# Performance work log

Measured on AMD Instinct MI355X. Metric: run time of the kernel, lower is better.

The kernel has to match this reference:

```python
import jax, jax.numpy as jnp
from jax import lax
import numpy as np

BETA, TAU, NUM_ITER = 0.33, 1.0, 5
DN = ('NCDHW', 'OIDHW', 'NCDHW')


def _base_kernels():
    # 3x3x3 neighborhood-counting kernels from the torch module
    K_N6 = np.zeros((3, 3, 3), np.float32)
    for c in [(1, 1, 0), (1, 1, 2), (1, 0, 1), (1, 2, 1), (0, 1, 1), (2, 1, 1)]:
        K_N6[c] = 1.0
    K_N26 = np.ones((3, 3, 3), np.float32); K_N26[1, 1, 1] = 0.0
    K_N18 = K_N26.copy()
    for c in [(0, 0, 0), (0, 0, 2), (0, 2, 0), (0, 2, 2), (2, 0, 0), (2, 0, 2), (2, 2, 0), (2, 2, 2)]:
        K_N18[c] = 0.0
    K_B26 = np.zeros((3, 3, 3), np.float32)
    K_B26[0, 0, 0] = 1.0
    for c in [(0, 0, 1), (0, 1, 0), (0, 1, 1), (1, 0, 0), (1, 0, 1), (1, 1, 0)]:
        K_B26[c] = -1.0
    K_A6 = np.zeros((3, 3, 3), np.float32)
    K_A6[0, 1, 1] = -1.0
    for c in [(0, 0, 1), (0, 1, 0), (0, 1, 2), (0, 2, 1)]:
        K_A6[c] = 1.0
    return K_N6, K_N26, K_N18, K_B26, K_A6


def _stacked_weight():
    # Fuse all 17 simple-check convolutions into one conv over a 3-channel input
    # channel 0: img, channel 1: 1-img, channel 2: 2*img-1
    K_N6, K_N26, K_N18, K_B26, K_A6 = _base_kernels()
    b26 = [K_B26] + [np.flip(K_B26, ax) for ax in [(0,), (1,), (2,), (0, 1), (0, 2), (1, 2), (0, 1, 2)]]
    fA = np.flip(K_A6, 0)
    a6 = [K_A6, np.rot90(K_A6, axes=(0, 1)), np.rot90(K_A6, axes=(0, 2)),
          fA, np.rot90(fA, axes=(0, 1)), np.rot90(fA, axes=(0, 2))]
    rows = []
    def put(k, ch):
        w = np.zeros((3, 3, 3, 3), np.float32)
        w[ch] = k
        rows.append(w)
    put(K_N6, 1)   # counts bg 6-neighbors (applied to 1-img)
    put(K_N26, 0)  # counts fg 26-neighbors
    put(K_N18, 0)  # counts fg 18-neighbors
    for k in b26:
        put(k, 2)  # 8 B26-cell detectors on 2*img-1
    for k in a6:
        put(k, 2)  # 6 A6-cell detectors on 2*img-1
    return jnp.asarray(np.stack(rows)), jnp.asarray(K_N26).reshape(1, 1, 3, 3, 3)


W_SIMPLE, W_N26 = _stacked_weight()


def _clip01(x):  # F.hardtanh(x, 0, 1)
    return jnp.clip(x, 0.0, 1.0)


def _endpoint_check(img):
    p = jnp.pad(img, ((0, 0), (0, 0), (1, 1), (1, 1), (1, 1)))
    n26 = lax.conv_general_dilated(p, W_N26, (1, 1, 1), 'VALID', dimension_numbers=DN)
    return _clip01(2.0 - n26)  # endpoint iff <=1 fg 26-neighbor


def _simple_check(img):
    p = jnp.pad(img, ((0, 0), (0, 0), (1, 1), (1, 1), (1, 1)))
    x3 = jnp.concatenate([p, 1.0 - p, 2.0 * p - 1.0], axis=1)
    f = lax.conv_general_dilated(x3, W_SIMPLE, (2, 2, 2), 'VALID', dimension_numbers=DN)
    n6, n26, n18 = f[:, 0:1], f[:, 1:2], f[:, 2:3]
    num_b26 = jax.nn.relu(f[:, 3:11] - 6.0).sum(axis=1, keepdims=True)
    num_a6 = jax.nn.relu(f[:, 11:17] - 4.0).sum(axis=1, keepdims=True)
    cond1 = _clip01(n6) * _clip01(2.0 - n6)                              # exactly one bg 6-neighbor
    cond2 = _clip01(n26) * _clip01(2.0 - n26)                            # exactly one fg 26-neighbor
    cond3 = _clip01(n18) * _clip01(2.0 - n18) * _clip01(1.0 - num_b26)   # one 18-neighbor, no B26 cell
    cond4 = _clip01(n6 - 1.0) * _clip01(1.0 - num_a6) * _clip01(1.0 - num_b26)  # >=2 bg 6-nb, no A6/B26 cell
    return _clip01(cond1 + cond2 + cond3 + cond4)


def _forward(img):
    # _prepare_input: zero-pad each spatial dim by 1
    img = jnp.pad(img, ((0, 0), (0, 0), (1, 1), (1, 1), (1, 1)))
    # _stochastic_discretization (reparametrization + straight-through)
    alpha = (img + 1e-8) / (1.0 - img + 1e-8)
    u = jax.random.uniform(jax.random.key(42), img.shape, img.dtype, 1e-8, 1.0 - 1e-8)
    noise = jnp.log(u) - jnp.log1p(-u)
    soft = jax.nn.sigmoid((jnp.log(alpha) + noise * BETA) / TAU)
    img = lax.stop_gradient((soft > 0.5).astype(soft.dtype) - soft) + soft
    offsets = [(0, 0, 0), (1, 0, 0), (0, 1, 0), (1, 1, 0), (0, 0, 1), (1, 0, 1), (0, 1, 1), (1, 1, 1)]
    for _ in range(NUM_ITER):
        is_end = _endpoint_check(img)
        for xo, yo, zo in offsets:
            is_simple = _simple_check(img[:, :, xo:, yo:, zo:])
            sl = (slice(None), slice(None), slice(xo, None, 2), slice(yo, None, 2), slice(zo, None, 2))
            del_cand = is_simple * (1.0 - is_end[sl])
            img = img.at[sl].set(jnp.minimum(img[sl], 1.0 - del_cand))
    # _prepare_output: strip padding
    return img[:, :, 1:-1, 1:-1, 1:-1]


def setup_inputs():
    key = jax.random.key(0)
    img = jax.random.uniform(key, (2, 1, 160, 160, 160), jnp.float32)  # probabilities in [0,1)
    return {"img": img}


def reference(img):
    return _forward(img)
```

## Files before the change

kernel.cpp:

```cpp
#include <hip/hip_runtime.h>
#include <stdint.h>

#pragma clang fp contract(off)

#define PDIM 162
#define NW   (2*PDIM*PDIM*3)
#define NWH  (NW/2)
#define OD   160

#define PZ 97
#define LADDR(lz,ly) ((lz)*PZ + (ly)*3)

__device__ __forceinline__ uint32_t rotl32(uint32_t x, uint32_t r) {
  return (x << r) | (x >> (32u - r));
}

__device__ __forceinline__ uint32_t threefry_bits(uint32_t idx) {
  const uint32_t ks0 = 0u, ks1 = 42u, ks2 = 0x1BD11BDAu ^ 0u ^ 42u;
  uint32_t x0 = 0u + ks0;
  uint32_t x1 = idx + ks1;
#define TFR(r) { x0 += x1; x1 = rotl32(x1, (r)); x1 ^= x0; }
  TFR(13u) TFR(15u) TFR(26u) TFR(6u)
  x0 += ks1; x1 += ks2 + 1u;
  TFR(17u) TFR(29u) TFR(16u) TFR(24u)
  x0 += ks2; x1 += ks0 + 2u;
  TFR(13u) TFR(15u) TFR(26u) TFR(6u)
  x0 += ks0; x1 += ks1 + 3u;
  TFR(17u) TFR(29u) TFR(16u) TFR(24u)
  x0 += ks1; x1 += ks2 + 4u;
  TFR(13u) TFR(15u) TFR(26u) TFR(6u)
  x0 += ks2; x1 += ks0 + 5u;
#undef TFR
  return x0 ^ x1;
}

__device__ __forceinline__ float xla_logf(float xin) {
  uint32_t bits = __float_as_uint(xin);
  float e = (float)((int)(bits >> 23) - 126);
  float x = __uint_as_float((bits & 0x007fffffu) | 0x3f000000u);
  const float SQRTHF = 0.707106781186547524f;
  bool lt = (x < SQRTHF);
  float tmp = lt ? x : 0.0f;
  e = e - (lt ? 1.0f : 0.0f);
  x = x - 1.0f;
  x = x + tmp;
  float z = x * x;
  float y = 7.0376836292e-2f;
  y = fmaf(y, x, -1.1514610310e-1f);
  y = fmaf(y, x,  1.1676998740e-1f);
  y = fmaf(y, x, -1.2420140846e-1f);
  y = fmaf(y, x,  1.4249322787e-1f);
  y = fmaf(y, x, -1.6668057665e-1f);
  y = fmaf(y, x,  2.0000714765e-1f);
  y = fmaf(y, x, -2.4999993993e-1f);
  y = fmaf(y, x,  3.3333331174e-1f);
  y = y * x;
  y = y * z;
  y = fmaf(e, -2.12194440e-4f, y);
  y = fmaf(-0.5f, z, y);
  x = x + y;
  x = fmaf(e, 0.693359375f, x);
  return x;
}

__device__ __forceinline__ float xla_log1pf(float x) {
  float for_large = xla_logf(x + 1.0f);
  float for_small = fmaf(-0.5f, x, 1.0f) * x;
  return (fabsf(x) < 1e-4f) ? for_small : for_large;
}

__device__ __forceinline__ bool bin_pred(const float* __restrict__ in, uint32_t w,
                                         uint32_t lane) {
  uint32_t row = w / 3u, wx = w - row * 3u;
  uint32_t n  = row / (uint32_t)(PDIM * PDIM);
  uint32_t rr = row - n * (uint32_t)(PDIM * PDIM);
  uint32_t z  = rr / (uint32_t)PDIM;
  uint32_t y  = rr - z * (uint32_t)PDIM;
  uint32_t x  = wx * 64u + lane;
  if ((z - 1u) >= 160u || (y - 1u) >= 160u || (x - 1u) >= 160u) return false;
  float v = in[((n * 160u + (z - 1u)) * 160u + (y - 1u)) * 160u + (x - 1u)];
  uint32_t i = row * 162u + x;
  uint32_t b = threefry_bits(i);
  float f  = __uint_as_float((b >> 9) | 0x3f800000u) - 1.0f;
  float uu = fmaxf(1e-8f, f + 1e-8f);
  float h  = (v + 1e-8f) / ((1.0f - v) + 1e-8f);
  const float T = 1.1920928955078125e-7f;

  const float LN2 = 0.6931471805599453f;
  float la_f = __builtin_amdgcn_logf(h) * LN2;
  float nz_f = (__builtin_amdgcn_logf(uu) - __builtin_amdgcn_logf(1.0f - uu)) * LN2;
  float zs_f = fmaf(nz_f, 0.33f, la_f);
  if (fabsf(zs_f - T) > 3.0e-4f) return zs_f > T;

  float la = xla_logf(h);
  float noise = xla_logf(uu) - xla_log1pf(-uu);
  float zs = la + noise * 0.33f;
  return zs > T;
}

__global__ __launch_bounds__(256) void k_binarize(const float* __restrict__ in,
                                                  uint64_t* __restrict__ bits) {
  uint32_t t = blockIdx.x * 256u + threadIdx.x;
  uint32_t w0 = t >> 6, lane = t & 63u;
  if (w0 >= (uint32_t)NWH) return;
  uint32_t w1 = w0 + (uint32_t)NWH;
  bool p0 = bin_pred(in, w0, lane);
  bool p1 = bin_pred(in, w1, lane);
  uint64_t m0 = __ballot(p0);
  uint64_t m1 = __ballot(p1);
  if (lane == 0) { bits[w0] = m0; bits[w1] = m1; }
}

#define NB(dz,dy,dx) ((dx)==-1 ? Lb[(dz)+1][(dy)+1] : ((dx)==1 ? Rb[(dz)+1][(dy)+1] : Vv[(dz)+1][(dy)+1]))

#define GATHER_W(SRC, lz, ly, w) \
  _Pragma("unroll") \
  for (int dz = 0; dz < 3; ++dz) \
    _Pragma("unroll") \
    for (int dy = 0; dy < 3; ++dy) { \
      int rb = LADDR((lz) + dz - 1, (ly) + dy - 1); \
      uint64_t r0 = SRC[rb], r1 = SRC[rb + 1], r2 = SRC[rb + 2]; \
      uint64_t b = ((w) == 0) ? r0 : (((w) == 1) ? r1 : r2); \
      uint64_t a = ((w) == 0) ? 0ull : (((w) == 1) ? r0 : r1); \
      uint64_t d = ((w) == 0) ? r1 : (((w) == 1) ? r2 : 0ull); \
      Vv[dz][dy] = b; \
      Lb[dz][dy] = (b << 1) | (a >> 63); \
      Rb[dz][dy] = (b >> 1) | (d << 63); \
    }

struct OG { uint64_t o, g; };
__device__ __forceinline__ OG og_leaf2(uint64_t a, uint64_t b) {
  OG r; r.o = a | b; r.g = a & b; return r;
}
__device__ __forceinline__ OG og_comb(OG a, OG b) {
  OG r; r.g = a.g | b.g | (a.o & b.o); r.o = a.o | b.o; return r;
}

#define OG_BUILD_18_C(og18, ogc) \
  OG a0 = og_leaf2(NB(-1,0,0), NB(1,0,0)); \
  OG a1 = og_leaf2(NB(0,-1,0), NB(0,1,0)); \
  OG a2 = og_leaf2(NB(0,0,-1), NB(0,0,1)); \
  OG e0 = og_leaf2(NB(-1,-1,0), NB(-1,1,0)); \
  OG e1 = og_leaf2(NB(-1,0,-1), NB(-1,0,1)); \
  OG e2 = og_leaf2(NB(1,-1,0),  NB(1,1,0)); \
  OG e3 = og_leaf2(NB(1,0,-1),  NB(1,0,1)); \
  OG e4 = og_leaf2(NB(0,-1,-1), NB(0,-1,1)); \
  OG e5 = og_leaf2(NB(0,1,-1),  NB(0,1,1)); \
  OG t0 = og_comb(a0, a1); \
  OG t1 = og_comb(a2, e0); \
  OG t2 = og_comb(e1, e2); \
  OG t3 = og_comb(e3, e4); \
  OG og18 = og_comb(og_comb(og_comb(t0, t1), og_comb(t2, t3)), e5); \
  OG c0 = og_leaf2(NB(-1,-1,-1), NB(-1,-1,1)); \
  OG c1 = og_leaf2(NB(-1,1,-1),  NB(-1,1,1)); \
  OG c2 = og_leaf2(NB(1,-1,-1),  NB(1,-1,1)); \
  OG c3 = og_leaf2(NB(1,1,-1),   NB(1,1,1)); \
  OG ogc = og_comb(og_comb(c0, c1), og_comb(c2, c3));

__global__ __launch_bounds__(256) void k_ge2(const uint64_t* __restrict__ board,
                                             uint64_t* __restrict__ Ge) {
  int ti = blockIdx.x * 256 + threadIdx.x;
  int w = ti % 3;  int r = ti / 3;
  int y = 1 + (r % 160);  int rr = r / 160;
  int z = 1 + (rr % 160); int n = rr / 160;
  int idx = ((n * 162 + z) * 162 + y) * 3 + w;
  uint64_t res = 0;
  if (board[idx] != 0ull) {
    uint64_t Vv[3][3], Lb[3][3], Rb[3][3];
#pragma unroll
    for (int dz = 0; dz < 3; ++dz)
#pragma unroll
      for (int dy = 0; dy < 3; ++dy) {
        const uint64_t* p = board + ((n * 162 + z - 1 + dz) * 162 + (y - 1 + dy)) * 3;
        uint64_t r0 = p[0], r1 = p[1], r2 = p[2];
        uint64_t b = (w == 0) ? r0 : ((w == 1) ? r1 : r2);
        uint64_t a = (w == 0) ? 0ull : ((w == 1) ? r0 : r1);
        uint64_t d = (w == 0) ? r1 : ((w == 1) ? r2 : 0ull);
        Vv[dz][dy] = b;
        Lb[dz][dy] = (b << 1) | (a >> 63);
        Rb[dz][dy] = (b >> 1) | (d << 63);
      }
    OG_BUILD_18_C(og18, ogc)
    res = og_comb(og18, ogc).g;
  }
  Ge[idx] = res;
}

__global__ __launch_bounds__(1024) void k_iter(const uint64_t* __restrict__ bin,
                                               const uint64_t* __restrict__ gein,
                                               uint64_t* __restrict__ bout,
                                               float4* __restrict__ outf,
                                               int zero_pads) {
  __shared__ uint64_t Bt[32 * PZ];
  __shared__ uint64_t Gl[32 * PZ];
  const int tid = threadIdx.x;
  const int bid = blockIdx.x;
  const int n  = bid / 100;
  const int rm = bid - n * 100;
  const int tz = rm / 10, ty = rm - tz * 10;
  const int gz0 = 1 + 16 * tz, gy0 = 1 + 16 * ty;

  if (zero_pads && bid == 0) {
    for (int j = tid; j < 1288; j += 1024) {
      int nn, z, y;
      if (j < 648) { nn = j / 324; int r = j - nn * 324;
                     z = (r >= 162) ? 161 : 0; y = (r >= 162) ? r - 162 : r; }
      else { int j2 = j - 648; nn = j2 / 320; int r = j2 - nn * 320;
             y = (r >= 160) ? 161 : 0; z = 1 + ((r >= 160) ? r - 160 : r); }
      uint64_t* p = bout + (((nn * 162 + z) * 162) + y) * 3;
      p[0] = 0; p[1] = 0; p[2] = 0;
    }
  }

  for (int ti = tid; ti < 32 * 32 * 3; ti += 1024) {
    int w = ti % 3, r = ti / 3, ly = r % 32, lz = r / 32;
    int z = gz0 - 8 + lz, y = gy0 - 8 + ly;
    uint64_t v = 0;
    if ((unsigned)z < 162u && (unsigned)y < 162u)
      v = bin[((n * 162 + z) * 162 + y) * 3 + w];
    Bt[LADDR(lz, ly) + w] = v;
  }
  for (int ti = tid; ti < 30 * 30 * 3; ti += 1024) {
    int w = ti % 3, r = ti / 3, iy = r % 30, iz = r / 30;
    int z = gz0 - 7 + iz, y = gy0 - 7 + iy;
    uint64_t v = 0;
    if ((unsigned)(z - 1) < 160u && (unsigned)(y - 1) < 160u)
      v = gein[((n * 162 + z) * 162 + y) * 3 + w];
    Gl[LADDR(1 + iz, 1 + iy) + w] = v;
  }
  __syncthreads();

  const int PLZ[8] = {1,0,1,0,1,0,1,0};
  const int PLY[8] = {1,1,0,0,1,1,0,0};
#pragma unroll
  for (int k = 0; k < 8; ++k) {
    const int h = 7 - k, cnt1 = 8 + h;
    const uint64_t xmask = (k < 4) ? 0x5555555555555555ull : 0xAAAAAAAAAAAAAAAAull;
    const int s0 = 8 - h;
    const int slz = s0 + ((s0 ^ PLZ[k]) & 1);
    const int sly = s0 + ((s0 ^ PLY[k]) & 1);
    for (int ti = tid; ti < cnt1 * cnt1 * 3; ti += 1024) {
      int w = ti % 3, r = ti / 3, iy = r % cnt1, iz = r / cnt1;
      int lz = slz + 2 * iz, ly = sly + 2 * iy;
      int base = LADDR(lz, ly) + w;
      uint64_t center = Bt[base];
      uint64_t act = center & xmask & Gl[base];
      if (act == 0ull) continue;
      uint64_t Vv[3][3], Lb[3][3], Rb[3][3];
      GATHER_W(Bt, lz, ly, w)

      OG_BUILD_18_C(og18, ogc)
      OG og26 = og_comb(og18, ogc);
      uint64_t e18 = og18.o & ~og18.g;
      uint64_t e26 = og26.o & ~og26.g;

      uint64_t m0f = ~NB(-1,0,0), m1f = ~NB(1,0,0), m2f = ~NB(0,-1,0);
      uint64_t m3f = ~NB(0,1,0),  m4f = ~NB(0,0,-1), m5f = ~NB(0,0,1);
      OG p0 = og_leaf2(m0f, m1f);
      OG p1 = og_leaf2(m2f, m3f);
      OG p2 = og_leaf2(m4f, m5f);
      OG pm = og_comb(og_comb(p0, p1), p2);
      uint64_t c6eq5 = pm.o & ~pm.g;
      uint64_t c6le4 = pm.g;

      uint64_t del = (c6eq5 | e26) & act;
      uint64_t need = act & ~del & (e18 | c6le4);
      if (need != 0ull) {
        uint64_t badB = 0;
#pragma unroll
        for (int sz = -1; sz <= 1; sz += 2)
#pragma unroll
          for (int sy = -1; sy <= 1; sy += 2)
#pragma unroll
            for (int sx = -1; sx <= 1; sx += 2) {
              uint64_t oct = NB(sz,0,0) | NB(0,sy,0) | NB(0,0,sx)
                           | NB(sz,sy,0) | NB(sz,0,sx) | NB(0,sy,sx);
              badB |= NB(sz,sy,sx) & ~oct;
            }
        uint64_t b0ok = ~badB;

        uint64_t badA = 0;
        badA |= ~NB(-1,0,0) & NB(-1,-1,0) & NB(-1,1,0) & NB(-1,0,-1) & NB(-1,0,1);
        badA |= ~NB( 1,0,0) & NB( 1,-1,0) & NB( 1,1,0) & NB( 1,0,-1) & NB( 1,0,1);
        badA |= ~NB(0,-1,0) & NB(-1,-1,0) & NB(1,-1,0) & NB(0,-1,-1) & NB(0,-1,1);
        badA |= ~NB(0, 1,0) & NB(-1, 1,0) & NB(1, 1,0) & NB(0, 1,-1) & NB(0, 1,1);
        badA |= ~NB(0,0,-1) & NB(-1,0,-1) & NB(1,0,-1) & NB(0,-1,-1) & NB(0,1,-1);
        badA |= ~NB(0,0, 1) & NB(-1,0, 1) & NB(1,0, 1) & NB(0,-1, 1) & NB(0,1, 1);
        uint64_t a0ok = ~badA;

        del |= ((e18 & b0ok) | (c6le4 & a0ok & b0ok)) & act;
      }
      if (del) Bt[base] = center & ~del;
    }
    __syncthreads();
  }

  if (outf) {
    for (int ti = tid; ti < 16 * 16 * 40; ti += 1024) {
      int g = ti % 40, r = ti / 40, iy = r % 16, iz = r / 16;
      int base = LADDR(8 + iz, 8 + iy);
      int bi = 1 + 4 * g;
      int wx = bi >> 6, sft = bi & 63;
      uint64_t v = Bt[base + wx] >> sft;
      if (sft > 60) v |= Bt[base + wx + 1] << (64 - sft);
      outf[((n * 160 + (gz0 + iz - 1)) * 160 + (gy0 + iy - 1)) * 40 + g] =
          make_float4((float)(v & 1u), (float)((v >> 1) & 1u),
                      (float)((v >> 2) & 1u), (float)((v >> 3) & 1u));
    }
  } else {
    for (int ti = tid; ti < 16 * 16 * 3; ti += 1024) {
      int w = ti % 3, r = ti / 3, iy = r % 16, iz = r / 16;
      bout[((n * 162 + gz0 + iz) * 162 + (gy0 + iy)) * 3 + w] =
          Bt[LADDR(8 + iz, 8 + iy) + w];
    }
  }
}

extern "C" void kernel_launch(void* const* d_in, const int* in_sizes, int n_in,
                              void* d_out, int out_size, void* d_ws, size_t ws_size,
                              hipStream_t stream) {
  const float* in = (const float*)d_in[0];
  float4* out = (float4*)d_out;
  uint64_t* A = (uint64_t*)d_ws;
  uint64_t* B = A + NW;
  uint64_t* G = B + NW;

  k_binarize<<<dim3((NWH * 64 + 255) / 256), dim3(256), 0, stream>>>(in, A);

  k_ge2<<<dim3(600), dim3(256), 0, stream>>>(A, G);
  k_iter<<<dim3(200), dim3(1024), 0, stream>>>(A, G, B, nullptr, 1);
  k_ge2<<<dim3(600), dim3(256), 0, stream>>>(B, G);
  k_iter<<<dim3(200), dim3(1024), 0, stream>>>(B, G, A, nullptr, 0);
  k_ge2<<<dim3(600), dim3(256), 0, stream>>>(A, G);
  k_iter<<<dim3(200), dim3(1024), 0, stream>>>(A, G, B, nullptr, 0);
  k_ge2<<<dim3(600), dim3(256), 0, stream>>>(B, G);
  k_iter<<<dim3(200), dim3(1024), 0, stream>>>(B, G, A, nullptr, 0);
  k_ge2<<<dim3(600), dim3(256), 0, stream>>>(A, G);
  k_iter<<<dim3(200), dim3(1024), 0, stream>>>(A, G, nullptr, out, 0);
}
```

Before: 216.7 us.

## Fuse next-iteration endpoint mask computation into k_iter epilogue

```diff
diff --git a/kernel.cpp b/kernel.cpp
--- a/kernel.cpp
+++ b/kernel.cpp
@@ -8,7 +8,10 @@
 #define NWH  (NW/2)
 #define OD   160
 
-#define PZ 97
+#define HALO 9
+#define TZ 34
+#define TY 34
+#define PZ 103
 #define LADDR(lz,ly) ((lz)*PZ + (ly)*3)
 
 __device__ __forceinline__ uint32_t rotl32(uint32_t x, uint32_t r) {
@@ -189,10 +192,11 @@
 __global__ __launch_bounds__(1024) void k_iter(const uint64_t* __restrict__ bin,
                                                const uint64_t* __restrict__ gein,
                                                uint64_t* __restrict__ bout,
+                                               uint64_t* __restrict__ gout,
                                                float4* __restrict__ outf,
                                                int zero_pads) {
-  __shared__ uint64_t Bt[32 * PZ];
-  __shared__ uint64_t Gl[32 * PZ];
+  __shared__ uint64_t Bt[TZ * PZ];
+  __shared__ uint64_t Gl[TZ * PZ];
   const int tid = threadIdx.x;
   const int bid = blockIdx.x;
   const int n  = bid / 100;
@@ -212,31 +216,32 @@
     }
   }
 
-  for (int ti = tid; ti < 32 * 32 * 3; ti += 1024) {
-    int w = ti % 3, r = ti / 3, ly = r % 32, lz = r / 32;
-    int z = gz0 - 8 + lz, y = gy0 - 8 + ly;
+  for (int ti = tid; ti < TZ * TY * 3; ti += 1024) {
+    int w = ti % 3, r = ti / 3, ly = r % TY, lz = r / TY;
+    int z = gz0 - HALO + lz, y = gy0 - HALO + ly;
     uint64_t v = 0;
     if ((unsigned)z < 162u && (unsigned)y < 162u)
       v = bin[((n * 162 + z) * 162 + y) * 3 + w];
     Bt[LADDR(lz, ly) + w] = v;
   }
-  for (int ti = tid; ti < 30 * 30 * 3; ti += 1024) {
-    int w = ti % 3, r = ti / 3, iy = r % 30, iz = r / 30;
-    int z = gz0 - 7 + iz, y = gy0 - 7 + iy;
+  for (int ti = tid; ti < 32 * 32 * 3; ti += 1024) {
+    int w = ti % 3, r = ti / 3, iy = r % 32, iz = r / 32;
+    int lz = 1 + iz, ly = 1 + iy;
+    int z = gz0 - 8 + iz, y = gy0 - 8 + iy;
     uint64_t v = 0;
     if ((unsigned)(z - 1) < 160u && (unsigned)(y - 1) < 160u)
       v = gein[((n * 162 + z) * 162 + y) * 3 + w];
-    Gl[LADDR(1 + iz, 1 + iy) + w] = v;
+    Gl[LADDR(lz, ly) + w] = v;
   }
   __syncthreads();
 
-  const int PLZ[8] = {1,0,1,0,1,0,1,0};
-  const int PLY[8] = {1,1,0,0,1,1,0,0};
+  const int PLZ[8] = {0,1,0,1,0,1,0,1};
+  const int PLY[8] = {0,0,1,1,0,0,1,1};
 #pragma unroll
   for (int k = 0; k < 8; ++k) {
-    const int h = 7 - k, cnt1 = 8 + h;
+    const int h2 = 8 - k, cnt1 = 8 + h2;
     const uint64_t xmask = (k < 4) ? 0x5555555555555555ull : 0xAAAAAAAAAAAAAAAAull;
-    const int s0 = 8 - h;
+    const int s0 = HALO - h2;
     const int slz = s0 + ((s0 ^ PLZ[k]) & 1);
     const int sly = s0 + ((s0 ^ PLY[k]) & 1);
     for (int ti = tid; ti < cnt1 * cnt1 * 3; ti += 1024) {
@@ -295,10 +300,26 @@
     __syncthreads();
   }
 
+  if (gout) {
+    for (int ti = tid; ti < 16 * 16 * 3; ti += 1024) {
+      int w = ti % 3, r = ti / 3, iy = r % 16, iz = r / 16;
+      int lz = HALO + iz, ly = HALO + iy;
+      int base = LADDR(lz, ly) + w;
+      uint64_t res = 0;
+      if (Bt[base] != 0ull) {
+        uint64_t Vv[3][3], Lb[3][3], Rb[3][3];
+        GATHER_W(Bt, lz, ly, w)
+        OG_BUILD_18_C(og18, ogc)
+        res = og_comb(og18, ogc).g;
+      }
+      gout[((n * 162 + gz0 + iz) * 162 + (gy0 + iy)) * 3 + w] = res;
+    }
+  }
+
   if (outf) {
     for (int ti = tid; ti < 16 * 16 * 40; ti += 1024) {
       int g = ti % 40, r = ti / 40, iy = r % 16, iz = r / 16;
-      int base = LADDR(8 + iz, 8 + iy);
+      int base = LADDR(HALO + iz, HALO + iy);
       int bi = 1 + 4 * g;
       int wx = bi >> 6, sft = bi & 63;
       uint64_t v = Bt[base + wx] >> sft;
@@ -311,7 +332,7 @@
     for (int ti = tid; ti < 16 * 16 * 3; ti += 1024) {
       int w = ti % 3, r = ti / 3, iy = r % 16, iz = r / 16;
       bout[((n * 162 + gz0 + iz) * 162 + (gy0 + iy)) * 3 + w] =
-          Bt[LADDR(8 + iz, 8 + iy) + w];
+          Bt[LADDR(HALO + iz, HALO + iy) + w];
     }
   }
 }
@@ -321,20 +342,16 @@
                               hipStream_t stream) {
   const float* in = (const float*)d_in[0];
   float4* out = (float4*)d_out;
-  uint64_t* A = (uint64_t*)d_ws;
-  uint64_t* B = A + NW;
-  uint64_t* G = B + NW;
+  uint64_t* A  = (uint64_t*)d_ws;
+  uint64_t* B  = A + NW;
+  uint64_t* G0 = B + NW;
+  uint64_t* G1 = G0 + NW;
 
   k_binarize<<<dim3((NWH * 64 + 255) / 256), dim3(256), 0, stream>>>(in, A);
-
-  k_ge2<<<dim3(600), dim3(256), 0, stream>>>(A, G);
-  k_iter<<<dim3(200), dim3(1024), 0, stream>>>(A, G, B, nullptr, 1);
-  k_ge2<<<dim3(600), dim3(256), 0, stream>>>(B, G);
-  k_iter<<<dim3(200), dim3(1024), 0, stream>>>(B, G, A, nullptr, 0);
-  k_ge2<<<dim3(600), dim3(256), 0, stream>>>(A, G);
-  k_iter<<<dim3(200), dim3(1024), 0, stream>>>(A, G, B, nullptr, 0);
-  k_ge2<<<dim3(600), dim3(256), 0, stream>>>(B, G);
-  k_iter<<<dim3(200), dim3(1024), 0, stream>>>(B, G, A, nullptr, 0);
-  k_ge2<<<dim3(600), dim3(256), 0, stream>>>(A, G);
-  k_iter<<<dim3(200), dim3(1024), 0, stream>>>(A, G, nullptr, out, 0);
-}
+  k_ge2<<<dim3(600), dim3(256), 0, stream>>>(A, G0);
+  k_iter<<<dim3(200), dim3(1024), 0, stream>>>(A, G0, B, G1, nullptr, 1);
+  k_iter<<<dim3(200), dim3(1024), 0, stream>>>(B, G1, A, G0, nullptr, 0);
+  k_iter<<<dim3(200), dim3(1024), 0, stream>>>(A, G0, B, G1, nullptr, 0);
+  k_iter<<<dim3(200), dim3(1024), 0, stream>>>(B, G1, A, G0, nullptr, 0);
+  k_iter<<<dim3(200), dim3(1024), 0, stream>>>(A, G0, nullptr, nullptr, out, 0);
+}
```

Result: no change. 217.2 us (+0.2%).
